# Kernel optimization log

Hardware: AMD Instinct MI355X
Metric: run time of the kernel (lower is better)

## Reference

```python
import jax, jax.numpy as jnp
import numpy as np

# Dimensions: T total prefill tokens, S ragged segments (one adapter each),
# M target modules sharing this linear, r LoRA rank.
T, D_IN, D_OUT, R, M, S = 8192, 4096, 4096, 16, 2, 8


def setup_inputs() -> dict:
    key = jax.random.key(0)
    ks = jax.random.split(key, 6)
    x = jax.random.normal(ks[0], (T, D_IN), dtype=jnp.float32)
    W = jax.random.normal(ks[1], (D_OUT, D_IN), dtype=jnp.float32) * 0.02
    b = jax.random.normal(ks[2], (D_OUT,), dtype=jnp.float32) * 0.02
    # lora_A[m, s] = A.T of adapter s for target module m: [D_IN, R]
    lora_A = jax.random.normal(ks[3], (M, S, D_IN, R), dtype=jnp.float32) * 0.02
    # lora_B[m, s] = B.T: [R, D_OUT]
    lora_B = jax.random.normal(ks[4], (M, S, R, D_OUT), dtype=jnp.float32) * 0.02
    cu = jnp.sort(jax.random.randint(ks[5], (S + 1,), 0, T + 1, dtype=jnp.int32))
    cu = cu.at[0].set(0).at[-1].set(T)  # segment boundaries cover [0, T)
    return {"x": x, "W": W, "b": b, "lora_A": lora_A, "lora_B": lora_B,
            "cu_seqlen": cu}


def reference(x, W, b, lora_A, lora_B, cu_seqlen):
    # Base linear: out = x @ W.T + b
    out = x @ W.T + b
    tok = jnp.arange(x.shape[0])
    n_seg = lora_A.shape[1]
    # SGMV-style ragged LoRA: tokens in segment s use adapter s for every
    # target module m; contributions from all modules add into `out`.
    # Masking (instead of dynamic slicing) keeps shapes static / jit-friendly
    # and is exact: masked-out tokens contribute zero.
    for s in range(n_seg):
        mask = ((tok >= cu_seqlen[s]) & (tok < cu_seqlen[s + 1]))
        xm = x * mask.astype(x.dtype)[:, None]            # [T, D_IN], zero outside segment
        u = jnp.einsum('td,mdr->tmr', xm, lora_A[:, s])    # [T, M, R] low-rank down-proj
        out = out + jnp.einsum('tmr,mrD->tD', u, lora_B[:, s])  # up-proj, sum over modules
    return out
```

## Files before the change

kernel.cpp:

```cpp
#include <hip/hip_runtime.h>
#include <hip/hip_bf16.h>

#define T_TOK 8192
#define DIN   4096
#define DOUT  4096
#define RANK  16
#define NMOD  2
#define NSEG  8

typedef __attribute__((ext_vector_type(8))) short bf16x8;
typedef __attribute__((ext_vector_type(8))) unsigned short u16x8;
typedef __attribute__((ext_vector_type(4))) float f32x4;

__device__ inline unsigned short f2bf(float f) {
    union { float f; unsigned u; } v; v.f = f;
    unsigned r = v.u + 0x7FFFu + ((v.u >> 16) & 1u);
    return (unsigned short)(r >> 16);
}

__device__ inline void gload_lds16(const void* g, void* l) {
    __builtin_amdgcn_global_load_lds(
        (const __attribute__((address_space(1))) void*)g,
        (__attribute__((address_space(3))) void*)l, 16, 0, 0);
}

__global__ void cast_bf16_kernel(const float* __restrict__ src,
                                 unsigned short* __restrict__ dst, int n8) {
    int i = blockIdx.x * blockDim.x + threadIdx.x;
    if (i >= n8) return;
    const float4* s4 = (const float4*)src;
    float4 a = s4[2 * (size_t)i];
    float4 b = s4[2 * (size_t)i + 1];
    u16x8 o;
    o[0] = f2bf(a.x); o[1] = f2bf(a.y); o[2] = f2bf(a.z); o[3] = f2bf(a.w);
    o[4] = f2bf(b.x); o[5] = f2bf(b.y); o[6] = f2bf(b.z); o[7] = f2bf(b.w);
    *(u16x8*)(dst + 8 * (size_t)i) = o;
}

__global__ void prep_A_kernel(const float* __restrict__ A,
                              unsigned short* __restrict__ At) {
    int idx = blockIdx.x * 256 + threadIdx.x;
    int d   = idx & (DIN - 1);
    int smr = idx >> 12;
    int s   = smr >> 5, mr = smr & 31;
    int m   = mr >> 4,  r  = mr & 15;
    float v = A[(((size_t)(m * NSEG + s) * DIN) + d) * RANK + r];
    At[idx] = f2bf(v);
}

__global__ void prep_B_kernel(const float* __restrict__ B,
                              unsigned short* __restrict__ Bt) {
    int o  = blockIdx.x * 256 + threadIdx.x;
    int s  = o >> 12;
    int oc = o & (DOUT - 1);
    unsigned short tmp[32];
    for (int m = 0; m < NMOD; ++m)
        for (int r = 0; r < RANK; ++r)
            tmp[m * 16 + r] =
                f2bf(B[(((size_t)(m * NSEG + s) * RANK) + r) * DOUT + oc]);
    for (int k = 0; k < 4; ++k) {
        u16x8 v;
        for (int j = 0; j < 8; ++j) v[j] = tmp[k * 8 + j];
        *(u16x8*)(Bt + (size_t)o * 32 + k * 8) = v;
    }
}

__global__ __launch_bounds__(64) void u_gemm_kernel(
    const unsigned short* __restrict__ xb, const unsigned short* __restrict__ At,
    const int* __restrict__ cu, float* __restrict__ Pu) {
    int tile = blockIdx.x;
    int ky   = blockIdx.y;
    int lane = threadIdx.x;
    int l15  = lane & 15, lk = lane >> 4;
    int t0   = tile * 32;
    f32x4 acc[2][2] = {};
    bf16x8 zero = {};
    for (int s = 0; s < NSEG; ++s) {
        int lo = cu[s], hi = cu[s + 1];
        if (hi <= t0 || lo >= t0 + 32) continue;
        const unsigned short* atb = At + (size_t)(s * 32) * DIN;
        for (int kt = 0; kt < 32; ++kt) {
            int k0 = ky * 1024 + kt * 32 + lk * 8;
            bf16x8 a[2], b[2];
            for (int mi = 0; mi < 2; ++mi) {
                int row = t0 + mi * 16 + l15;
                bf16x8 av = *(const bf16x8*)(xb + (size_t)row * DIN + k0);
                a[mi] = (row >= lo && row < hi) ? av : zero;
            }
            for (int ni = 0; ni < 2; ++ni) {
                int mr = ni * 16 + l15;
                b[ni] = *(const bf16x8*)(atb + (size_t)mr * DIN + k0);
            }
            for (int mi = 0; mi < 2; ++mi)
                for (int ni = 0; ni < 2; ++ni)
                    acc[mi][ni] = __builtin_amdgcn_mfma_f32_16x16x32_bf16(
                        a[mi], b[ni], acc[mi][ni], 0, 0, 0);
        }
    }
    for (int mi = 0; mi < 2; ++mi)
        for (int ni = 0; ni < 2; ++ni)
            for (int j = 0; j < 4; ++j) {
                int t  = t0 + mi * 16 + lk * 4 + j;
                int mr = ni * 16 + l15;
                Pu[((size_t)ky * T_TOK + t) * 32 + mr] = acc[mi][ni][j];
            }
}

__global__ void reduce_u_kernel(const float* __restrict__ Pu,
                                unsigned short* __restrict__ ub) {
    int idx = blockIdx.x * 256 + threadIdx.x;
    const size_t STRIDE = (size_t)T_TOK * 32;
    float s = Pu[idx] + Pu[idx + STRIDE] + Pu[idx + 2 * STRIDE] + Pu[idx + 3 * STRIDE];
    ub[idx] = f2bf(s);
}


__device__ __forceinline__ bf16x8 lds_frag(const char* tile, int row, int lk) {
    int rb = (row << 6) + (lk << 4);
    rb ^= ((rb >> 7) & 7) << 4;
    return *(const bf16x8*)(tile + rb);
}

__device__ __forceinline__ void stage_chunk(const unsigned short* gbase,
                                            char* lds_tile, int chunkbase, int tid) {
    int tb = chunkbase + tid * 16;
    int gb = tb ^ (((tb >> 7) & 7) << 4);
    int row = gb >> 6;
    int col = (gb & 63) >> 1;
    gload_lds16(gbase + (size_t)row * DIN + col, lds_tile + tb);
}

#define KTILE_BODY(T_, STG_, VM_)                                              \
  {                                                                            \
    const int t_ = (T_);                                                       \
    const char* Asl = lds + (t_ & 3) * 32768;                                  \
    const char* Bsl = Asl + 16384;                                             \
    bf16x8 bfr[4], af[4];                                                      \
    for (int n = 0; n < 4; ++n)                                                \
        bfr[n] = lds_frag(Bsl, wcol + n * 16 + l15, lk);                       \
    for (int m = 0; m < 4; ++m)                                                \
        af[m] = lds_frag(Asl, wrow + m * 16 + l15, lk);                        \
    if (STG_) {                                                                \
        int k0s = (t_ + 3) * 32;                                               \
        char* dst = lds + ((t_ + 3) & 3) * 32768;                              \
        stage_chunk(xrow + k0s, dst, 0, tid);                                  \
        stage_chunk(xrow + k0s, dst, 8192, tid);                               \
    }                                                                          \
    __builtin_amdgcn_s_setprio(1);                                             \
    for (int m = 0; m < 4; ++m)                                                \
        for (int n = 0; n < 4; ++n)                                            \
            acc[m][n] = __builtin_amdgcn_mfma_f32_16x16x32_bf16(               \
                af[m], bfr[n], acc[m][n], 0, 0, 0);                            \
    __builtin_amdgcn_s_setprio(0);                                             \
    for (int m = 0; m < 4; ++m)                                                \
        af[m] = lds_frag(Asl, wrow + (4 + m) * 16 + l15, lk);                  \
    if (STG_) {                                                                \
        int k0s = (t_ + 3) * 32;                                               \
        char* dst = lds + ((t_ + 3) & 3) * 32768 + 16384;                      \
        stage_chunk(wrow_g + k0s, dst, 0, tid);                                \
        stage_chunk(wrow_g + k0s, dst, 8192, tid);                             \
    }                                                                          \
    __builtin_amdgcn_s_setprio(1);                                             \
    for (int m = 0; m < 4; ++m)                                                \
        for (int n = 0; n < 4; ++n)                                            \
            acc[4 + m][n] = __builtin_amdgcn_mfma_f32_16x16x32_bf16(           \
                af[m], bfr[n], acc[4 + m][n], 0, 0, 0);                        \
    __builtin_amdgcn_s_setprio(0);                                             \
    if ((VM_) == 8)      asm volatile("s_waitcnt vmcnt(8)" ::: "memory");      \
    else if ((VM_) == 4) asm volatile("s_waitcnt vmcnt(4)" ::: "memory");      \
    else if ((VM_) == 0) asm volatile("s_waitcnt vmcnt(0)" ::: "memory");      \
    if ((VM_) >= 0) __builtin_amdgcn_s_barrier();                              \
  }

__global__ __launch_bounds__(512, 2) void main_gemm_kernel(
    const unsigned short* __restrict__ xb, const unsigned short* __restrict__ wb,
    const unsigned short* __restrict__ ub, const unsigned short* __restrict__ bt,
    const float* __restrict__ bias, const int* __restrict__ cu,
    float* __restrict__ out) {
    __shared__ __attribute__((aligned(1024))) char lds[131072];
    int tid  = threadIdx.x;
    int w    = tid >> 6, lane = tid & 63;
    int l15  = lane & 15, lk = lane >> 4;
    int wrow = (w >> 2) * 128;
    int wcol = (w & 3) * 64;
    int swz  = (blockIdx.x & 7) * 64 + (blockIdx.x >> 3);
    int row0 = (swz >> 4) * 256;
    int col0 = (swz & 15) * 256;

    const unsigned short* xrow   = xb + (size_t)row0 * DIN;
    const unsigned short* wrow_g = wb + (size_t)col0 * DIN;

    f32x4 acc[8][4] = {};

    for (int pt = 0; pt < 3; ++pt) {
        int k0s = pt * 32;
        char* slot = lds + pt * 32768;
        stage_chunk(xrow + k0s, slot, 0, tid);
        stage_chunk(xrow + k0s, slot, 8192, tid);
        stage_chunk(wrow_g + k0s, slot + 16384, 0, tid);
        stage_chunk(wrow_g + k0s, slot + 16384, 8192, tid);
    }
    asm volatile("s_waitcnt vmcnt(8)" ::: "memory");
    __builtin_amdgcn_s_barrier();

    #pragma unroll 1
    for (int t = 0; t < 125; ++t) KTILE_BODY(t, 1, 8);
    KTILE_BODY(125, 0, 4);
    KTILE_BODY(126, 0, 0);
    KTILE_BODY(127, 0, -1);

    bf16x8 zero = {};
    for (int s = 0; s < NSEG; ++s) {
        int lo = cu[s], hi = cu[s + 1];
        if (hi <= row0 || lo >= row0 + 256) continue;
        bf16x8 au[8], bu[4];
        for (int m = 0; m < 8; ++m) {
            int row = row0 + wrow + m * 16 + l15;
            bf16x8 v = *(const bf16x8*)(ub + (size_t)row * 32 + lk * 8);
            au[m] = (row >= lo && row < hi) ? v : zero;
        }
        for (int n = 0; n < 4; ++n) {
            int col = col0 + wcol + n * 16 + l15;
            bu[n] = *(const bf16x8*)(bt + ((size_t)s * DOUT + col) * 32 + lk * 8);
        }
        for (int m = 0; m < 8; ++m)
            for (int n = 0; n < 4; ++n)
                acc[m][n] = __builtin_amdgcn_mfma_f32_16x16x32_bf16(
                    au[m], bu[n], acc[m][n], 0, 0, 0);
    }

    float bv[4];
    for (int n = 0; n < 4; ++n) bv[n] = bias[col0 + wcol + n * 16 + l15];
    for (int m = 0; m < 8; ++m) {
        int rbase = row0 + wrow + m * 16 + lk * 4;
        for (int n = 0; n < 4; ++n) {
            int col = col0 + wcol + n * 16 + l15;
            for (int jj = 0; jj < 4; ++jj)
                out[(size_t)(rbase + jj) * DOUT + col] = acc[m][n][jj] + bv[n];
        }
    }
}

extern "C" void kernel_launch(void* const* d_in, const int* in_sizes, int n_in,
                              void* d_out, int out_size, void* d_ws, size_t ws_size,
                              hipStream_t stream) {
    const float* x  = (const float*)d_in[0];
    const float* W  = (const float*)d_in[1];
    const float* b  = (const float*)d_in[2];
    const float* lA = (const float*)d_in[3];
    const float* lB = (const float*)d_in[4];
    const int*   cu = (const int*)d_in[5];
    float* out = (float*)d_out;

    char* ws = (char*)d_ws;
    unsigned short* xb = (unsigned short*)(ws);
    unsigned short* wb = (unsigned short*)(ws + 67108864);
    unsigned short* At = (unsigned short*)(ws + 100663296);
    unsigned short* Bt = (unsigned short*)(ws + 102760448);
    float*          Pu = (float*)(ws + 104857600);
    unsigned short* ub = (unsigned short*)(ws + 109051904);

    cast_bf16_kernel<<<(T_TOK * DIN / 8) / 256, 256, 0, stream>>>(x, xb, T_TOK * DIN / 8);
    cast_bf16_kernel<<<(DOUT * DIN / 8) / 256, 256, 0, stream>>>(W, wb, DOUT * DIN / 8);
    prep_A_kernel<<<(NSEG * 32 * DIN) / 256, 256, 0, stream>>>(lA, At);
    prep_B_kernel<<<(NSEG * DOUT) / 256, 256, 0, stream>>>(lB, Bt);
    dim3 ug(T_TOK / 32, 4);
    u_gemm_kernel<<<ug, 64, 0, stream>>>(xb, At, cu, Pu);
    reduce_u_kernel<<<(T_TOK * 32) / 256, 256, 0, stream>>>(Pu, ub);
    dim3 mg(32 * 16);
    main_gemm_kernel<<<mg, 512, 0, stream>>>(xb, wb, ub, Bt, b, cu, out);
}
```

Measured before the change: 333.0 us.

## Software-pipeline LDS fragment reads across k-tiles and merge the bf16 cast launches

Restructures the main GEMM k-loop so the next tile's B and A fragments are read from LDS into double-buffered registers while the current tile's MFMAs run. Each tile's global-to-LDS staging is issued in one group, with one wait and one barrier per iteration and sched_barrier fences to keep the compiler's order. Separately, the x and W fp32-to-bf16 casts are merged into one launch. Holding two register fragment sets raises register pressure under the 512x2 launch bounds, and the new vmcnt counts and slot reuse must stay correct.

New measurement: 326.6 us. No clear change (-1.9%).

```diff
diff --git a/kernel.cpp b/kernel.cpp
--- a/kernel.cpp
+++ b/kernel.cpp
@@ -24,17 +24,24 @@
         (__attribute__((address_space(3))) void*)l, 16, 0, 0);
 }
 
-__global__ void cast_bf16_kernel(const float* __restrict__ src,
-                                 unsigned short* __restrict__ dst, int n8) {
+__global__ void cast2_bf16_kernel(const float* __restrict__ sa,
+                                  unsigned short* __restrict__ da, int n8a,
+                                  const float* __restrict__ sb,
+                                  unsigned short* __restrict__ db, int n8b) {
     int i = blockIdx.x * blockDim.x + threadIdx.x;
-    if (i >= n8) return;
-    const float4* s4 = (const float4*)src;
-    float4 a = s4[2 * (size_t)i];
-    float4 b = s4[2 * (size_t)i + 1];
+    const float* s;
+    unsigned short* d;
+    size_t j;
+    if (i < n8a) { s = sa; d = da; j = (size_t)i; }
+    else if (i < n8a + n8b) { s = sb; d = db; j = (size_t)(i - n8a); }
+    else return;
+    const float4* s4 = (const float4*)s;
+    float4 a = s4[2 * j];
+    float4 b = s4[2 * j + 1];
     u16x8 o;
     o[0] = f2bf(a.x); o[1] = f2bf(a.y); o[2] = f2bf(a.z); o[3] = f2bf(a.w);
     o[4] = f2bf(b.x); o[5] = f2bf(b.y); o[6] = f2bf(b.z); o[7] = f2bf(b.w);
-    *(u16x8*)(dst + 8 * (size_t)i) = o;
+    *(u16x8*)(d + 8 * j) = o;
 }
 
 __global__ void prep_A_kernel(const float* __restrict__ A,
@@ -130,44 +137,55 @@
     gload_lds16(gbase + (size_t)row * DIN + col, lds_tile + tb);
 }
 
-#define KTILE_BODY(T_, STG_, VM_)                                              \
-  {                                                                            \
-    const int t_ = (T_);                                                       \
-    const char* Asl = lds + (t_ & 3) * 32768;                                  \
-    const char* Bsl = Asl + 16384;                                             \
-    bf16x8 bfr[4], af[4];                                                      \
+#define STAGE(T_)                                                              \
+  {                                                                            \
+    int k0s_ = (T_) * 32;                                                      \
+    char* dst_ = lds + ((T_) & 3) * 32768;                                     \
+    stage_chunk(xrow + k0s_, dst_, 0, tid);                                    \
+    stage_chunk(xrow + k0s_, dst_, 8192, tid);                                 \
+    stage_chunk(wrow_g + k0s_, dst_ + 16384, 0, tid);                          \
+    stage_chunk(wrow_g + k0s_, dst_ + 16384, 8192, tid);                       \
+  }
+
+#define READ_AF2(T_)                                                           \
+  {                                                                            \
+    const char* Asl_ = lds + ((T_) & 3) * 32768;                               \
+    for (int m = 0; m < 4; ++m)                                                \
+        af2[m] = lds_frag(Asl_, wrow + (4 + m) * 16 + l15, lk);                \
+  }
+
+#define READ_MAIN(BFR_, AF_, T_)                                               \
+  {                                                                            \
+    const char* Asl_ = lds + ((T_) & 3) * 32768;                               \
+    const char* Bsl_ = Asl_ + 16384;                                           \
     for (int n = 0; n < 4; ++n)                                                \
-        bfr[n] = lds_frag(Bsl, wcol + n * 16 + l15, lk);                       \
-    for (int m = 0; m < 4; ++m)                                                \
-        af[m] = lds_frag(Asl, wrow + m * 16 + l15, lk);                        \
-    if (STG_) {                                                                \
-        int k0s = (t_ + 3) * 32;                                               \
-        char* dst = lds + ((t_ + 3) & 3) * 32768;                              \
-        stage_chunk(xrow + k0s, dst, 0, tid);                                  \
-        stage_chunk(xrow + k0s, dst, 8192, tid);                               \
-    }                                                                          \
+        BFR_[n] = lds_frag(Bsl_, wcol + n * 16 + l15, lk);                     \
+    for (int m = 0; m < 4; ++m)                                                \
+        AF_[m] = lds_frag(Asl_, wrow + m * 16 + l15, lk);                      \
+  }
+
+#define CLUSTER(BFR_, AF_)                                                     \
+  {                                                                            \
     __builtin_amdgcn_s_setprio(1);                                             \
     for (int m = 0; m < 4; ++m)                                                \
         for (int n = 0; n < 4; ++n)                                            \
             acc[m][n] = __builtin_amdgcn_mfma_f32_16x16x32_bf16(               \
-                af[m], bfr[n], acc[m][n], 0, 0, 0);                            \
-    __builtin_amdgcn_s_setprio(0);                                             \
-    for (int m = 0; m < 4; ++m)                                                \
-        af[m] = lds_frag(Asl, wrow + (4 + m) * 16 + l15, lk);                  \
-    if (STG_) {                                                                \
-        int k0s = (t_ + 3) * 32;                                               \
-        char* dst = lds + ((t_ + 3) & 3) * 32768 + 16384;                      \
-        stage_chunk(wrow_g + k0s, dst, 0, tid);                                \
-        stage_chunk(wrow_g + k0s, dst, 8192, tid);                             \
-    }                                                                          \
-    __builtin_amdgcn_s_setprio(1);                                             \
+                AF_[m], BFR_[n], acc[m][n], 0, 0, 0);                          \
     for (int m = 0; m < 4; ++m)                                                \
         for (int n = 0; n < 4; ++n)                                            \
             acc[4 + m][n] = __builtin_amdgcn_mfma_f32_16x16x32_bf16(           \
-                af[m], bfr[n], acc[4 + m][n], 0, 0, 0);                        \
+                af2[m], BFR_[n], acc[4 + m][n], 0, 0, 0);                      \
     __builtin_amdgcn_s_setprio(0);                                             \
-    if ((VM_) == 8)      asm volatile("s_waitcnt vmcnt(8)" ::: "memory");      \
-    else if ((VM_) == 4) asm volatile("s_waitcnt vmcnt(4)" ::: "memory");      \
+  }
+
+#define ITER(UB_, UA_, RB_, RA_, T_, STG_, VM_)                                \
+  {                                                                            \
+    READ_AF2(T_);                                                              \
+    READ_MAIN(RB_, RA_, (T_) + 1);                                             \
+    if (STG_) STAGE((T_) + 3);                                                 \
+    __builtin_amdgcn_sched_barrier(0);                                         \
+    CLUSTER(UB_, UA_);                                                         \
+    if ((VM_) == 4)      asm volatile("s_waitcnt vmcnt(4)" ::: "memory");      \
     else if ((VM_) == 0) asm volatile("s_waitcnt vmcnt(0)" ::: "memory");      \
     if ((VM_) >= 0) __builtin_amdgcn_s_barrier();                              \
   }
@@ -191,23 +209,22 @@
     const unsigned short* wrow_g = wb + (size_t)col0 * DIN;
 
     f32x4 acc[8][4] = {};
-
-    for (int pt = 0; pt < 3; ++pt) {
-        int k0s = pt * 32;
-        char* slot = lds + pt * 32768;
-        stage_chunk(xrow + k0s, slot, 0, tid);
-        stage_chunk(xrow + k0s, slot, 8192, tid);
-        stage_chunk(wrow_g + k0s, slot + 16384, 0, tid);
-        stage_chunk(wrow_g + k0s, slot + 16384, 8192, tid);
-    }
-    asm volatile("s_waitcnt vmcnt(8)" ::: "memory");
+    bf16x8 bfrA[4], afA[4], bfrB[4], afB[4], af2[4];
+
+    STAGE(0); STAGE(1); STAGE(2);
+    asm volatile("s_waitcnt vmcnt(4)" ::: "memory");
     __builtin_amdgcn_s_barrier();
+    READ_MAIN(bfrA, afA, 0);
 
     #pragma unroll 1
-    for (int t = 0; t < 125; ++t) KTILE_BODY(t, 1, 8);
-    KTILE_BODY(125, 0, 4);
-    KTILE_BODY(126, 0, 0);
-    KTILE_BODY(127, 0, -1);
+    for (int t = 0; t < 124; t += 2) {
+        ITER(bfrA, afA, bfrB, afB, t,     1, 4);
+        ITER(bfrB, afB, bfrA, afA, t + 1, 1, 4);
+    }
+    ITER(bfrA, afA, bfrB, afB, 124, 1, 4);
+    ITER(bfrB, afB, bfrA, afA, 125, 0, 0);
+    ITER(bfrA, afA, bfrB, afB, 126, 0, -1);
+    { READ_AF2(127); __builtin_amdgcn_sched_barrier(0); CLUSTER(bfrB, afB); }
 
     bf16x8 zero = {};
     for (int s = 0; s < NSEG; ++s) {
@@ -260,8 +277,8 @@
     float*          Pu = (float*)(ws + 104857600);
     unsigned short* ub = (unsigned short*)(ws + 109051904);
 
-    cast_bf16_kernel<<<(T_TOK * DIN / 8) / 256, 256, 0, stream>>>(x, xb, T_TOK * DIN / 8);
-    cast_bf16_kernel<<<(DOUT * DIN / 8) / 256, 256, 0, stream>>>(W, wb, DOUT * DIN / 8);
+    const int n8x = T_TOK * DIN / 8, n8w = DOUT * DIN / 8;
+    cast2_bf16_kernel<<<(n8x + n8w) / 256, 256, 0, stream>>>(x, xb, n8x, W, wb, n8w);
     prep_A_kernel<<<(NSEG * 32 * DIN) / 256, 256, 0, stream>>>(lA, At);
     prep_B_kernel<<<(NSEG * DOUT) / 256, 256, 0, stream>>>(lB, Bt);
     dim3 ug(T_TOK / 32, 4);
```
